# Performance work log

Measured on AMD Instinct MI355X. Metric: run time of the kernel, lower is better.

The kernel has to match this reference:

```python
import jax, jax.numpy as jnp
import numpy as np

MAX_ATOMS = 14  # hard-coded padded atom slots per residue in the original module


def setup_inputs() -> dict:
    key = jax.random.key(0)
    k1, k2, k3 = jax.random.split(key, 3)
    N_RES = 100000
    C = 128  # config.m; OutputLayer(3) emits m channels, fc1 = Linear(14*m, 1)
    feature = jax.random.normal(k1, (N_RES * MAX_ATOMS, C), dtype=jnp.float32)
    atom_num = jax.random.randint(k2, (N_RES,), 0, MAX_ATOMS, dtype=jnp.int32)
    label_binary = jax.random.randint(k3, (N_RES,), 0, 2, dtype=jnp.int32)
    return {"feature": feature, "atom_num": atom_num, "label_binary": label_binary}


def reference(feature, atom_num, label_binary):
    # Ragged gather-to-padded: atoms of residue r live at flat positions
    # [offset[r], offset[r]+atom_num[r]) in `feature`; copy into slot [r, :atom_num[r], :]
    # of a zero-padded [N_res, 14, C] tensor (the original nested Python loop).
    counts = atom_num.astype(jnp.int32)
    offsets = jnp.concatenate([jnp.zeros((1,), jnp.int32), jnp.cumsum(counts)[:-1]])  # [N_res]
    slots = jnp.arange(MAX_ATOMS, dtype=jnp.int32)                                    # [14]
    idx = offsets[:, None] + slots[None, :]                                           # [N_res, 14]
    mask = slots[None, :] < counts[:, None]                                           # [N_res, 14]
    idx = jnp.clip(idx, 0, feature.shape[0] - 1)
    padded = feature[idx] * mask[:, :, None].astype(feature.dtype)                    # [N_res, 14, C]
    aa_feature = padded.reshape(padded.shape[0], -1)                                  # [N_res, 14*C]
    return aa_feature, label_binary
```

## Files before the change

kernel.cpp:

```cpp
#include <hip/hip_runtime.h>


#define MAX_ATOMS 14
#define CCH 128
#define F4_PER_ROW 32
#define F4_PER_RES (MAX_ATOMS * F4_PER_ROW)
#define RPB 16
#define RES_PER_WAVE 4

typedef float f32x4 __attribute__((ext_vector_type(4)));

__global__ __launch_bounds__(256) void k_sums(const int* __restrict__ atom_num,
                                              int n, int* __restrict__ sums) {
    __shared__ int lds[256];
    int t = threadIdx.x;
    int r = blockIdx.x * 256 + t;
    lds[t] = (r < n) ? atom_num[r] : 0;
    __syncthreads();
    for (int d = 128; d > 0; d >>= 1) {
        if (t < d) lds[t] += lds[t + d];
        __syncthreads();
    }
    if (t == 0) sums[blockIdx.x] = lds[0];
}

__global__ __launch_bounds__(256) void k_gather(
        const f32x4* __restrict__ feat,
        const int* __restrict__ atom_num,
        const int* __restrict__ sums,
        const int* __restrict__ label,
        f32x4* __restrict__ out,
        float* __restrict__ out_label,
        int n) {
    __shared__ int red[256];
    __shared__ int off_s[RPB];
    __shared__ int cnt_s[RPB];
    int t = threadIdx.x;
    int rbase = blockIdx.x * RPB;
    int c      = rbase >> 8;
    int j0     = rbase & 255;
    int chunk0 = c << 8;

    int part = 0;
    for (int j = t; j < c; j += 256) part += sums[j];
    if (t < j0) part += atom_num[chunk0 + t];
    red[t] = part;
    __syncthreads();
    for (int d = 128; d > 0; d >>= 1) {
        if (t < d) red[t] += red[t + d];
        __syncthreads();
    }
    int base = red[0];

    if (t < RPB) {
        int r = rbase + t;
        cnt_s[t] = (r < n) ? atom_num[r] : 0;
        if (r < n) out_label[r] = (float)label[r];
    }
    __syncthreads();
    if (t < RPB) {
        int o = base;
        #pragma unroll
        for (int i = 0; i < RPB; ++i) o += (i < t) ? cnt_s[i] : 0;
        off_s[t] = o;
    }
    __syncthreads();

    int wv   = t >> 6;
    int lane = t & 63;
    int halfrow = lane >> 5;

    for (int j = 0; j < RES_PER_WAVE; ++j) {
        int rl = wv * RES_PER_WAVE + j;
        int r  = rbase + rl;
        if (r >= n) break;
        int off = off_s[rl];
        int cnt = cnt_s[rl];
        const f32x4* fp = feat + (size_t)off * F4_PER_ROW + lane;
        f32x4* op = out + (size_t)r * F4_PER_RES + lane;
        #pragma unroll
        for (int i = 0; i < 7; ++i) {
            f32x4 v = (f32x4)0.f;
            if (2 * i + halfrow < cnt)
                v = __builtin_nontemporal_load(fp + i * 64);
            __builtin_nontemporal_store(v, op + i * 64);
        }
    }
}

extern "C" void kernel_launch(void* const* d_in, const int* in_sizes, int n_in,
                              void* d_out, int out_size, void* d_ws, size_t ws_size,
                              hipStream_t stream) {
    const float* feature = (const float*)d_in[0];
    const int* atom_num  = (const int*)d_in[1];
    const int* label     = (const int*)d_in[2];
    const int n = in_sizes[1];

    float* out = (float*)d_out;
    float* out_label = out + (size_t)n * MAX_ATOMS * CCH;

    int* ws_sums = (int*)d_ws;

    int nb = (n + 255) / 256;
    k_sums<<<nb, 256, 0, stream>>>(atom_num, n, ws_sums);

    int gb = (n + RPB - 1) / RPB;
    k_gather<<<gb, 256, 0, stream>>>((const f32x4*)feature, atom_num,
                                     ws_sums, label,
                                     (f32x4*)out, out_label, n);
}
```

Before: 220.1 us.

## Precompute per-residue offsets in a scan kernel and use persistent gather

Moves the exclusive prefix scan of atom counts out of the gather kernel into a separate prep kernel that writes per-residue offsets and labels to workspace. The gather becomes a grid-stride persistent kernel of 512 blocks × 1024 threads, one residue per wave, with no LDS reductions or barriers. This removes the redundant per-block reduction over earlier chunk sums, at the cost of an extra kernel launch and an extra offsets array round trip.

```diff
diff --git a/kernel.cpp b/kernel.cpp
--- a/kernel.cpp
+++ b/kernel.cpp
@@ -2,11 +2,11 @@
 
 
 #define MAX_ATOMS 14
-#define CCH 128
 #define F4_PER_ROW 32
 #define F4_PER_RES (MAX_ATOMS * F4_PER_ROW)
-#define RPB 16
-#define RES_PER_WAVE 4
+#define TILE 16
+#define GBLOCKS 512
+#define GTHREADS 1024
 
 typedef float f32x4 __attribute__((ext_vector_type(4)));
 
@@ -24,26 +24,18 @@
     if (t == 0) sums[blockIdx.x] = lds[0];
 }
 
-__global__ __launch_bounds__(256) void k_gather(
-        const f32x4* __restrict__ feat,
-        const int* __restrict__ atom_num,
-        const int* __restrict__ sums,
-        const int* __restrict__ label,
-        f32x4* __restrict__ out,
-        float* __restrict__ out_label,
-        int n) {
+__global__ __launch_bounds__(256) void k_prep(const int* __restrict__ atom_num,
+                                              const int* __restrict__ sums,
+                                              const int* __restrict__ label,
+                                              int n,
+                                              int* __restrict__ offsets,
+                                              float* __restrict__ out_label) {
     __shared__ int red[256];
-    __shared__ int off_s[RPB];
-    __shared__ int cnt_s[RPB];
+    __shared__ int scn[256];
     int t = threadIdx.x;
-    int rbase = blockIdx.x * RPB;
-    int c      = rbase >> 8;
-    int j0     = rbase & 255;
-    int chunk0 = c << 8;
-
+    int b = blockIdx.x;
     int part = 0;
-    for (int j = t; j < c; j += 256) part += sums[j];
-    if (t < j0) part += atom_num[chunk0 + t];
+    for (int j = t; j < b; j += 256) part += sums[j];
     red[t] = part;
     __syncthreads();
     for (int d = 128; d > 0; d >>= 1) {
@@ -51,39 +43,46 @@
         __syncthreads();
     }
     int base = red[0];
+    int r = b * 256 + t;
+    int v = (r < n) ? atom_num[r] : 0;
+    scn[t] = v;
+    __syncthreads();
+    for (int d = 1; d < 256; d <<= 1) {
+        int add = (t >= d) ? scn[t - d] : 0;
+        __syncthreads();
+        scn[t] += add;
+        __syncthreads();
+    }
+    if (r < n) {
+        offsets[r] = base + scn[t] - v;
+        out_label[r] = (float)label[r];
+    }
+}
 
-    if (t < RPB) {
-        int r = rbase + t;
-        cnt_s[t] = (r < n) ? atom_num[r] : 0;
-        if (r < n) out_label[r] = (float)label[r];
-    }
-    __syncthreads();
-    if (t < RPB) {
-        int o = base;
-        #pragma unroll
-        for (int i = 0; i < RPB; ++i) o += (i < t) ? cnt_s[i] : 0;
-        off_s[t] = o;
-    }
-    __syncthreads();
-
-    int wv   = t >> 6;
-    int lane = t & 63;
+__global__ __launch_bounds__(GTHREADS, 8) void k_gather(
+        const f32x4* __restrict__ feat,
+        const int* __restrict__ atom_num,
+        const int* __restrict__ offsets,
+        f32x4* __restrict__ out,
+        int n, int ntiles) {
+    int w       = threadIdx.x >> 6;
+    int lane    = threadIdx.x & 63;
     int halfrow = lane >> 5;
 
-    for (int j = 0; j < RES_PER_WAVE; ++j) {
-        int rl = wv * RES_PER_WAVE + j;
-        int r  = rbase + rl;
-        if (r >= n) break;
-        int off = off_s[rl];
-        int cnt = cnt_s[rl];
-        const f32x4* fp = feat + (size_t)off * F4_PER_ROW + lane;
-        f32x4* op = out + (size_t)r * F4_PER_RES + lane;
-        #pragma unroll
-        for (int i = 0; i < 7; ++i) {
-            f32x4 v = (f32x4)0.f;
-            if (2 * i + halfrow < cnt)
-                v = __builtin_nontemporal_load(fp + i * 64);
-            __builtin_nontemporal_store(v, op + i * 64);
+    for (int tile = blockIdx.x; tile < ntiles; tile += GBLOCKS) {
+        int r = tile * TILE + w;
+        if (r < n) {
+            int off = offsets[r];
+            int cnt = atom_num[r];
+            const f32x4* fp = feat + (size_t)off * F4_PER_ROW + lane;
+            f32x4* op = out + (size_t)r * F4_PER_RES + lane;
+            #pragma unroll
+            for (int i = 0; i < 7; ++i) {
+                f32x4 v = (f32x4)0.f;
+                if (2 * i + halfrow < cnt)
+                    v = __builtin_nontemporal_load(fp + i * 64);
+                __builtin_nontemporal_store(v, op + i * 64);
+            }
         }
     }
 }
@@ -97,15 +96,18 @@
     const int n = in_sizes[1];
 
     float* out = (float*)d_out;
-    float* out_label = out + (size_t)n * MAX_ATOMS * CCH;
-
-    int* ws_sums = (int*)d_ws;
+    float* out_label = out + (size_t)n * MAX_ATOMS * 128;
 
     int nb = (n + 255) / 256;
+    int* ws_sums    = (int*)d_ws;
+    int* ws_offsets = ws_sums + nb;
+
     k_sums<<<nb, 256, 0, stream>>>(atom_num, n, ws_sums);
+    k_prep<<<nb, 256, 0, stream>>>(atom_num, ws_sums, label, n,
+                                   ws_offsets, out_label);
 
-    int gb = (n + RPB - 1) / RPB;
-    k_gather<<<gb, 256, 0, stream>>>((const f32x4*)feature, atom_num,
-                                     ws_sums, label,
-                                     (f32x4*)out, out_label, n);
+    int ntiles = (n + TILE - 1) / TILE;
+    k_gather<<<GBLOCKS, GTHREADS, 0, stream>>>(
+        (const f32x4*)feature, atom_num, ws_offsets,
+        (f32x4*)out, n, ntiles);
 }
```

Result: faster. 206.9 us, median of 3 (-6.0%).
